# Optimization experiments

Measured on AMD Instinct MI355X. Metric: run time of the kernel, lower is better.

Reference implementation:

```python
import jax, jax.numpy as jnp
import numpy as np

B, T, C, H = 4, 2048, 768, 12
HD = C // H  # 64
EPS = 1e-5


def layer_norm(x, g, b):
    mu = jnp.mean(x, axis=-1, keepdims=True)
    var = jnp.var(x, axis=-1, keepdims=True)
    return (x - mu) * jax.lax.rsqrt(var + EPS) * g + b


def setup_inputs() -> dict:
    key = jax.random.key(0)
    ks = jax.random.split(key, 14)
    s_c = 1.0 / np.sqrt(C)
    s_4c = 1.0 / np.sqrt(4 * C)
    return {
        "x": jax.random.normal(ks[0], (B, T, C), jnp.float32),
        # per-head Q/K/V projections stacked over heads [H, C, HD]
        "wq": jax.random.uniform(ks[1], (H, C, HD), jnp.float32, -s_c, s_c),
        "bq": jnp.zeros((H, HD), jnp.float32),
        "wk": jax.random.uniform(ks[2], (H, C, HD), jnp.float32, -s_c, s_c),
        "bk": jnp.zeros((H, HD), jnp.float32),
        "wv": jax.random.uniform(ks[3], (H, C, HD), jnp.float32, -s_c, s_c),
        "bv": jnp.zeros((H, HD), jnp.float32),
        "w_proj": jax.random.uniform(ks[4], (C, C), jnp.float32, -s_c, s_c),
        "b_proj": jnp.zeros((C,), jnp.float32),
        "w1": jax.random.uniform(ks[5], (C, 4 * C), jnp.float32, -s_c, s_c),
        "b1": jnp.zeros((4 * C,), jnp.float32),
        "w2": jax.random.uniform(ks[6], (4 * C, C), jnp.float32, -s_4c, s_4c),
        "b2": jnp.zeros((C,), jnp.float32),
        "g1": jnp.ones((C,), jnp.float32),
        "beta1": jnp.zeros((C,), jnp.float32),
        "g2": jnp.ones((C,), jnp.float32),
        "beta2": jnp.zeros((C,), jnp.float32),
    }


def reference(x, wq, bq, wk, bk, wv, bv, w_proj, b_proj, w1, b1, w2, b2, g1, beta1, g2, beta2):
    # --- attention sublayer ---
    h = layer_norm(x, g1, beta1)
    q = jnp.einsum('btc,hcd->bhtd', h, wq) + bq[None, :, None, :]
    k = jnp.einsum('btc,hcd->bhtd', h, wk) + bk[None, :, None, :]
    v = jnp.einsum('btc,hcd->bhtd', h, wv) + bv[None, :, None, :]
    # NOTE: source applies NO 1/sqrt(head_size) scaling
    scores = jnp.einsum('bhtd,bhsd->bhts', q, k)  # [B,H,T,T]
    causal = jnp.tril(jnp.ones((T, T), bool))
    scores = jnp.where(causal, scores, -jnp.inf)
    wei = jax.nn.softmax(scores, axis=-1)
    attn = jnp.einsum('bhts,bhsd->bhtd', wei, v)  # [B,H,T,HD]
    attn = attn.transpose(0, 2, 1, 3).reshape(B, T, C)  # concat heads
    x = x + attn @ w_proj + b_proj
    # --- MLP sublayer ---
    h2 = layer_norm(x, g2, beta2)
    x = x + jax.nn.relu(h2 @ w1 + b1) @ w2 + b2
    return x
```

## Files before the change

### kernel.cpp

```cpp
#include <hip/hip_runtime.h>
#include <hip/hip_bf16.h>
#include <math.h>

#define BB 4
#define TT 2048
#define CC 768
#define HH 12
#define HDIM 64
#define C4 3072
#define MM (BB*TT)
#define EPSL 1e-5f

typedef __bf16 bf16x8 __attribute__((ext_vector_type(8)));
typedef float f32x4 __attribute__((ext_vector_type(4)));

__device__ __forceinline__ ushort f2bf(float f) {
    union { float f; unsigned u; } v; v.f = f;
    unsigned r = v.u + 0x7fffu + ((v.u >> 16) & 1u);
    return (ushort)(r >> 16);
}

__device__ __forceinline__ void glds16(const void* g, void* l) {
    __builtin_amdgcn_global_load_lds(
        (const __attribute__((address_space(1))) void*)g,
        (__attribute__((address_space(3))) void*)l, 16, 0, 0);
}

__global__ __launch_bounds__(256) void ln_k(const float* __restrict__ X,
                                            const float* __restrict__ G,
                                            const float* __restrict__ Be,
                                            ushort* __restrict__ O)
{
    int row = blockIdx.x;
    const float* xr = X + (size_t)row * CC;
    int t = threadIdx.x;
    float v0 = xr[t], v1 = xr[t + 256], v2 = xr[t + 512];
    float s  = v0 + v1 + v2;
    float sq = v0*v0 + v1*v1 + v2*v2;
    #pragma unroll
    for (int off = 32; off; off >>= 1) {
        s  += __shfl_xor(s,  off);
        sq += __shfl_xor(sq, off);
    }
    __shared__ float red[8];
    int wv = t >> 6, ln = t & 63;
    if (ln == 0) { red[wv] = s; red[4 + wv] = sq; }
    __syncthreads();
    s  = red[0] + red[1] + red[2] + red[3];
    sq = red[4] + red[5] + red[6] + red[7];
    float mu  = s * (1.0f / CC);
    float var = sq * (1.0f / CC) - mu * mu;
    float rs  = rsqrtf(var + EPSL);
    ushort* orow = O + (size_t)row * CC;
    orow[t]       = f2bf((v0 - mu) * rs * G[t]       + Be[t]);
    orow[t + 256] = f2bf((v1 - mu) * rs * G[t + 256] + Be[t + 256]);
    orow[t + 512] = f2bf((v2 - mu) * rs * G[t + 512] + Be[t + 512]);
}

template<int MODE>
__global__ __launch_bounds__(256) void repack_k(const float* __restrict__ W,
                                                ushort* __restrict__ WT,
                                                int K, int N, int outStride)
{
    __shared__ float tl[64][65];
    int n0 = blockIdx.x * 64, k0 = blockIdx.y * 64;
    int c = threadIdx.x & 63, rr = threadIdx.x >> 6;
    #pragma unroll
    for (int i = 0; i < 16; ++i) {
        int r = i * 4 + rr;
        float v;
        if (MODE == 0) v = W[(size_t)(k0 + r) * N + n0 + c];
        else           v = W[((size_t)(n0 >> 6) * CC + k0 + r) * 64 + c];
        tl[r][c] = v;
    }
    __syncthreads();
    #pragma unroll
    for (int i = 0; i < 16; ++i) {
        int r = i * 4 + rr;
        WT[(size_t)(n0 + r) * outStride + k0 + c] = f2bf(tl[c][r]);
    }
}

template<int EPI>
__global__ __launch_bounds__(256) void gemm_bf16(
    const ushort* __restrict__ A, const ushort* __restrict__ BT,
    int M, int N, int K,
    void* __restrict__ ov0, void* __restrict__ ov1, void* __restrict__ ov2,
    const float* __restrict__ bias0, const float* __restrict__ bias1,
    const float* __restrict__ bias2,
    const float* __restrict__ resid, ushort* __restrict__ obf)
{
    __shared__ ushort Al[128 * 32];
    __shared__ ushort Bl[128 * 32];
    int nbx = gridDim.x;
    int nwg = nbx * gridDim.y;
    int orig = blockIdx.y * nbx + blockIdx.x;
    int swz = orig;
    if ((nwg & 7) == 0) { int cpx = nwg >> 3; swz = (orig & 7) * cpx + (orig >> 3); }
    int bn = swz % nbx, bm = swz / nbx;

    int tid = threadIdx.x;
    int lane = tid & 63;
    int w = tid >> 6;
    int wr = (w >> 1) * 64, wc = (w & 1) * 64;
    int fr = lane & 15, kh = lane >> 4;

    f32x4 acc[4][4] = {};

    const size_t aRow = (size_t)bm * 128;
    const size_t bRow = (size_t)bn * 128;

    for (int k0 = 0; k0 < K; k0 += 32) {
        #pragma unroll
        for (int r = 0; r < 2; ++r) {
            int e = r * 256 + tid;
            glds16(A  + (aRow + (e >> 2)) * K + k0 + (e & 3) * 8, Al + e * 8);
            glds16(BT + (bRow + (e >> 2)) * K + k0 + (e & 3) * 8, Bl + e * 8);
        }
        __syncthreads();
        bf16x8 av[4], bv[4];
        #pragma unroll
        for (int i = 0; i < 4; ++i)
            av[i] = *(const bf16x8*)&Al[(wr + i * 16 + fr) * 32 + kh * 8];
        #pragma unroll
        for (int i = 0; i < 4; ++i)
            bv[i] = *(const bf16x8*)&Bl[(wc + i * 16 + fr) * 32 + kh * 8];
        #pragma unroll
        for (int i = 0; i < 4; ++i)
            #pragma unroll
            for (int j = 0; j < 4; ++j)
                acc[i][j] = __builtin_amdgcn_mfma_f32_16x16x32_bf16(av[i], bv[j], acc[i][j], 0, 0, 0);
        __syncthreads();
    }

    if (EPI == 1) {
        int seg = (bn * 128) / CC;
        ushort* op = (ushort*)(seg == 0 ? ov0 : (seg == 1 ? ov1 : ov2));
        const float* bsp = seg == 0 ? bias0 : (seg == 1 ? bias1 : bias2);
        int cb = bn * 128 - seg * CC + wc;
        int h = cb >> 6;
        #pragma unroll
        for (int i = 0; i < 4; ++i) {
            int row0 = bm * 128 + wr + i * 16 + kh * 4;
            int b = row0 >> 11;
            int t0 = row0 & (TT - 1);
            #pragma unroll
            for (int j = 0; j < 4; ++j) {
                int col = cb + j * 16 + fr;
                int d = col & 63;
                float bsv = bsp[col];
                #pragma unroll
                for (int r = 0; r < 4; ++r)
                    op[((size_t)(b * HH + h) * TT + t0 + r) * 64 + d] =
                        f2bf(acc[i][j][r] + bsv);
            }
        }
    } else if (EPI == 2) {
        float* o0 = (float*)ov0;
        int cb = bn * 128 + wc;
        #pragma unroll
        for (int i = 0; i < 4; ++i) {
            int row0 = bm * 128 + wr + i * 16 + kh * 4;
            #pragma unroll
            for (int j = 0; j < 4; ++j) {
                int col = cb + j * 16 + fr;
                float bsv = bias0[col];
                #pragma unroll
                for (int r = 0; r < 4; ++r) {
                    size_t idx = (size_t)(row0 + r) * N + col;
                    o0[idx] = acc[i][j][r] + bsv + resid[idx];
                }
            }
        }
    } else {
        int cb = bn * 128 + wc;
        #pragma unroll
        for (int i = 0; i < 4; ++i) {
            int row0 = bm * 128 + wr + i * 16 + kh * 4;
            #pragma unroll
            for (int j = 0; j < 4; ++j) {
                int col = cb + j * 16 + fr;
                float bsv = bias0[col];
                #pragma unroll
                for (int r = 0; r < 4; ++r) {
                    float v = fmaxf(acc[i][j][r] + bsv, 0.f);
                    obf[(size_t)(row0 + r) * N + col] = f2bf(v);
                }
            }
        }
    }
}

__global__ __launch_bounds__(256) void vtrans_k(const ushort* __restrict__ V,
                                                ushort* __restrict__ Vt)
{
    __shared__ ushort tl[64][72];
    int blk = blockIdx.x;
    int tt = blk & 31, bh = blk >> 5;
    size_t base = (size_t)bh * TT * 64;
    int t0 = tt * 64;
    int e = threadIdx.x;
    int rr = e >> 3, cc8 = (e & 7) * 8;
    #pragma unroll
    for (int p = 0; p < 2; ++p) {
        int t = p * 32 + rr;
        *(uint4*)&tl[t][cc8] = *(const uint4*)&V[base + (size_t)(t0 + t) * 64 + cc8];
    }
    __syncthreads();
    #pragma unroll
    for (int p = 0; p < 2; ++p) {
        int d = p * 32 + rr;
        ushort tmp[8];
        #pragma unroll
        for (int i = 0; i < 8; ++i) tmp[i] = tl[cc8 + i][d];
        *(uint4*)&Vt[base + (size_t)d * TT + t0 + cc8] = *(uint4*)tmp;
    }
}

__global__ __launch_bounds__(256) void attn_k(const ushort* __restrict__ Q,
                                              const ushort* __restrict__ Kb,
                                              const ushort* __restrict__ Vt,
                                              ushort* __restrict__ Ob)
{
    __shared__ ushort Kl[64][72];
    __shared__ ushort Vl[64][72];
    __shared__ ushort Pl[4][16][72];

    int orig = blockIdx.x;
    int swz = (orig & 7) * 96 + (orig >> 3);
    int pair = swz & 15;
    int bh = swz >> 4;
    int b = bh / HH, h = bh - b * HH;
    int tid = threadIdx.x, lane = tid & 63, w = tid >> 6;
    int c = lane & 15, g = lane >> 4;
    size_t base = (size_t)bh * TT * 64;
    int srow = tid >> 3, scol = (tid & 7) * 8;
    const float LOG2E = 1.44269504088896340736f;

    #pragma unroll
    for (int sel = 0; sel < 2; ++sel) {
        int qt = sel ? (31 - pair) : pair;
        int q0 = qt * 64;

        bf16x8 aq[2];
        #pragma unroll
        for (int kc = 0; kc < 2; ++kc) {
            bf16x8 raw = *(const bf16x8*)&Q[base + (size_t)(q0 + w * 16 + c) * 64 + kc * 32 + g * 8];
            #pragma unroll
            for (int e = 0; e < 8; ++e)
                raw[e] = (__bf16)((float)raw[e] * LOG2E);
            aq[kc] = raw;
        }

        f32x4 oa[4] = {};
        float mrun[4] = {-INFINITY, -INFINITY, -INFINITY, -INFINITY};
        float lrun[4] = {0.f, 0.f, 0.f, 0.f};

        for (int kv0 = 0; kv0 <= q0; kv0 += 64) {
            __syncthreads();
            #pragma unroll
            for (int p = 0; p < 2; ++p) {
                int r = p * 32 + srow;
                *(uint4*)&Kl[r][scol] = *(const uint4*)&Kb[base + (size_t)(kv0 + r) * 64 + scol];
                *(uint4*)&Vl[r][scol] = *(const uint4*)&Vt[base + (size_t)r * TT + kv0 + scol];
            }
            __syncthreads();

            f32x4 sa[4] = {};
            #pragma unroll
            for (int kc = 0; kc < 2; ++kc)
                #pragma unroll
                for (int j = 0; j < 4; ++j) {
                    bf16x8 kf = *(const bf16x8*)&Kl[j * 16 + c][kc * 32 + g * 8];
                    sa[j] = __builtin_amdgcn_mfma_f32_16x16x32_bf16(aq[kc], kf, sa[j], 0, 0, 0);
                }

            if (kv0 == q0) {
                #pragma unroll
                for (int j = 0; j < 4; ++j)
                    #pragma unroll
                    for (int r = 0; r < 4; ++r)
                        if (j * 16 + c > w * 16 + g * 4 + r) sa[j][r] = -1e30f;
            }

            float vlmax = sa[0][0];
            #pragma unroll
            for (int j = 0; j < 4; ++j)
                #pragma unroll
                for (int r = 0; r < 4; ++r) vlmax = fmaxf(vlmax, sa[j][r]);
            float mmin = fminf(fminf(mrun[0], mrun[1]), fminf(mrun[2], mrun[3]));
            if (!__all(vlmax <= mmin + 11.5f)) {
                #pragma unroll
                for (int r = 0; r < 4; ++r) {
                    float m0 = fmaxf(fmaxf(sa[0][r], sa[1][r]), fmaxf(sa[2][r], sa[3][r]));
                    #pragma unroll
                    for (int off = 8; off; off >>= 1) m0 = fmaxf(m0, __shfl_xor(m0, off));
                    float mnew = fmaxf(mrun[r], m0);
                    float sc = __builtin_amdgcn_exp2f(mrun[r] - mnew);
                    lrun[r] *= sc;
                    #pragma unroll
                    for (int j = 0; j < 4; ++j) oa[j][r] *= sc;
                    mrun[r] = mnew;
                }
            }
            #pragma unroll
            for (int r = 0; r < 4; ++r) {
                float ps = 0.f;
                #pragma unroll
                for (int j = 0; j < 4; ++j) {
                    float p = __builtin_amdgcn_exp2f(sa[j][r] - mrun[r]);
                    sa[j][r] = p;
                    ps += p;
                }
                lrun[r] += ps;
            }

            #pragma unroll
            for (int r = 0; r < 4; ++r)
                #pragma unroll
                for (int j = 0; j < 4; ++j)
                    Pl[w][g * 4 + r][j * 16 + c] = (ushort)__builtin_bit_cast(unsigned short, (__bf16)sa[j][r]);

            bf16x8 pf[2];
            #pragma unroll
            for (int kc = 0; kc < 2; ++kc)
                pf[kc] = *(const bf16x8*)&Pl[w][c][kc * 32 + g * 8];

            #pragma unroll
            for (int kc = 0; kc < 2; ++kc)
                #pragma unroll
                for (int j = 0; j < 4; ++j) {
                    bf16x8 vf = *(const bf16x8*)&Vl[j * 16 + c][kc * 32 + g * 8];
                    oa[j] = __builtin_amdgcn_mfma_f32_16x16x32_bf16(pf[kc], vf, oa[j], 0, 0, 0);
                }
        }

        float inv[4];
        #pragma unroll
        for (int r = 0; r < 4; ++r) {
            float l = lrun[r];
            #pragma unroll
            for (int off = 8; off; off >>= 1) l += __shfl_xor(l, off);
            inv[r] = 1.0f / l;
        }
        size_t orow = (size_t)b * TT + q0 + w * 16;
        #pragma unroll
        for (int j = 0; j < 4; ++j)
            #pragma unroll
            for (int r = 0; r < 4; ++r) {
                float v = oa[j][r] * inv[r];
                Ob[(orow + g * 4 + r) * CC + h * 64 + j * 16 + c] = f2bf(v);
            }
    }
}

extern "C" void kernel_launch(void* const* d_in, const int* in_sizes, int n_in,
                              void* d_out, int out_size, void* d_ws, size_t ws_size,
                              hipStream_t stream)
{
    const float* x   = (const float*)d_in[0];
    const float* wq  = (const float*)d_in[1];
    const float* bq  = (const float*)d_in[2];
    const float* wk  = (const float*)d_in[3];
    const float* bk  = (const float*)d_in[4];
    const float* wvw = (const float*)d_in[5];
    const float* bv  = (const float*)d_in[6];
    const float* wp  = (const float*)d_in[7];
    const float* bp  = (const float*)d_in[8];
    const float* w1  = (const float*)d_in[9];
    const float* b1  = (const float*)d_in[10];
    const float* w2  = (const float*)d_in[11];
    const float* b2  = (const float*)d_in[12];
    const float* g1  = (const float*)d_in[13];
    const float* be1 = (const float*)d_in[14];
    const float* g2  = (const float*)d_in[15];
    const float* be2 = (const float*)d_in[16];

    float* out = (float*)d_out;
    const size_t S = (size_t)MM * CC;

    ushort* wsu   = (ushort*)d_ws;
    ushort* WTqkv = wsu;
    ushort* WTp   = WTqkv + (size_t)2304 * 768;
    ushort* WT1   = WTp   + (size_t)768 * 768;
    ushort* WT2   = WT1   + (size_t)3072 * 768;
    ushort* hbf   = WT2   + (size_t)768 * 3072;
    ushort* attnb = hbf   + S;
    ushort* qb    = attnb + S;
    ushort* kb    = qb + S;
    ushort* vb    = kb + S;
    ushort* vtb   = vb + S;
    ushort* midb  = qb;

    dim3 rg(12, 12);
    repack_k<1><<<rg, 256, 0, stream>>>(wq,  WTqkv,                      768, 768, 768);
    repack_k<1><<<rg, 256, 0, stream>>>(wk,  WTqkv + (size_t)768*768,    768, 768, 768);
    repack_k<1><<<rg, 256, 0, stream>>>(wvw, WTqkv + (size_t)2*768*768,  768, 768, 768);
    repack_k<0><<<rg, 256, 0, stream>>>(wp,  WTp, 768, 768, 768);
    repack_k<0><<<dim3(48, 12), 256, 0, stream>>>(w1, WT1, 768, 3072, 768);
    repack_k<0><<<dim3(12, 48), 256, 0, stream>>>(w2, WT2, 3072, 768, 3072);

    ln_k<<<MM, 256, 0, stream>>>(x, g1, be1, hbf);
    gemm_bf16<1><<<dim3(18, 64), 256, 0, stream>>>(hbf, WTqkv, MM, 2304, CC,
        qb, kb, vb, bq, bk, bv, nullptr, nullptr);
    vtrans_k<<<48 * 32, 256, 0, stream>>>(vb, vtb);
    attn_k<<<48 * 16, 256, 0, stream>>>(qb, kb, vtb, attnb);
    gemm_bf16<2><<<dim3(6, 64), 256, 0, stream>>>(attnb, WTp, MM, CC, CC,
        out, nullptr, nullptr, bp, nullptr, nullptr, x, nullptr);

    ln_k<<<MM, 256, 0, stream>>>(out, g2, be2, hbf);
    gemm_bf16<3><<<dim3(24, 64), 256, 0, stream>>>(hbf, WT1, MM, C4, CC,
        nullptr, nullptr, nullptr, b1, nullptr, nullptr, nullptr, midb);
    gemm_bf16<2><<<dim3(6, 64), 256, 0, stream>>>(midb, WT2, MM, CC, C4,
        out, nullptr, nullptr, b2, nullptr, nullptr, out, nullptr);
}
```

Before: 313.6 us.

## Replace GEMM with 256x256 double-buffered 8-wave kernel using swizzled LDS

Replaces the 128x128 single-buffered bf16 GEMM with a 256x256 tile, 512-thread kernel that double-buffers K=64 slices in LDS. Each slice's global-to-LDS loads are interleaved with MFMA phases using explicit vmcnt waits and barriers. An XOR swizzle on LDS columns is meant to avoid bank conflicts. The goal is to hide global load latency behind compute and raise arithmetic intensity per tile. In exchange it uses a large LDS footprint (128KB per block), launches fewer workgroups (as few as 96 for the N=768 GEMMs, which can underfill the CUs), and relies on hand-tuned waitcnt ordering.

```diff
diff --git a/kernel.cpp b/kernel.cpp
--- a/kernel.cpp
+++ b/kernel.cpp
@@ -24,6 +24,15 @@
     __builtin_amdgcn_global_load_lds(
         (const __attribute__((address_space(1))) void*)g,
         (__attribute__((address_space(3))) void*)l, 16, 0, 0);
+}
+
+#define WVM(N) asm volatile("s_waitcnt vmcnt(" #N ")" ::: "memory")
+#define WLG0   asm volatile("s_waitcnt lgkmcnt(0)" ::: "memory")
+
+__device__ __forceinline__ void pbar() {
+    __builtin_amdgcn_sched_barrier(0);
+    __builtin_amdgcn_s_barrier();
+    __builtin_amdgcn_sched_barrier(0);
 }
 
 __global__ __launch_bounds__(256) void ln_k(const float* __restrict__ X,
@@ -82,7 +91,7 @@
 }
 
 template<int EPI>
-__global__ __launch_bounds__(256) void gemm_bf16(
+__global__ __launch_bounds__(512, 2) void gemm8p(
     const ushort* __restrict__ A, const ushort* __restrict__ BT,
     int M, int N, int K,
     void* __restrict__ ov0, void* __restrict__ ov1, void* __restrict__ ov2,
@@ -90,100 +99,152 @@
     const float* __restrict__ bias2,
     const float* __restrict__ resid, ushort* __restrict__ obf)
 {
-    __shared__ ushort Al[128 * 32];
-    __shared__ ushort Bl[128 * 32];
+    __shared__ ushort lds[2][2][256 * 64];
+
     int nbx = gridDim.x;
     int nwg = nbx * gridDim.y;
     int orig = blockIdx.y * nbx + blockIdx.x;
-    int swz = orig;
-    if ((nwg & 7) == 0) { int cpx = nwg >> 3; swz = (orig & 7) * cpx + (orig >> 3); }
+    int cpx = nwg >> 3;
+    int swz = (orig & 7) * cpx + (orig >> 3);
     int bn = swz % nbx, bm = swz / nbx;
 
     int tid = threadIdx.x;
     int lane = tid & 63;
     int w = tid >> 6;
-    int wr = (w >> 1) * 64, wc = (w & 1) * 64;
+    int wrow = (w >> 2) * 128, wcol = (w & 3) * 64;
     int fr = lane & 15, kh = lane >> 4;
-
-    f32x4 acc[4][4] = {};
-
-    const size_t aRow = (size_t)bm * 128;
-    const size_t bRow = (size_t)bn * 128;
-
-    for (int k0 = 0; k0 < K; k0 += 32) {
-        #pragma unroll
-        for (int r = 0; r < 2; ++r) {
-            int e = r * 256 + tid;
-            glds16(A  + (aRow + (e >> 2)) * K + k0 + (e & 3) * 8, Al + e * 8);
-            glds16(BT + (bRow + (e >> 2)) * K + k0 + (e & 3) * 8, Bl + e * 8);
-        }
-        __syncthreads();
-        bf16x8 av[4], bv[4];
-        #pragma unroll
-        for (int i = 0; i < 4; ++i)
-            av[i] = *(const bf16x8*)&Al[(wr + i * 16 + fr) * 32 + kh * 8];
-        #pragma unroll
-        for (int i = 0; i < 4; ++i)
-            bv[i] = *(const bf16x8*)&Bl[(wc + i * 16 + fr) * 32 + kh * 8];
-        #pragma unroll
-        for (int i = 0; i < 4; ++i)
-            #pragma unroll
-            for (int j = 0; j < 4; ++j)
-                acc[i][j] = __builtin_amdgcn_mfma_f32_16x16x32_bf16(av[i], bv[j], acc[i][j], 0, 0, 0);
-        __syncthreads();
+    int rxor = (fr & 7) * 8;
+
+    const size_t aR0 = (size_t)bm * 256;
+    const size_t bR0 = (size_t)bn * 256;
+    const int nt = K >> 6;
+
+    int srow = tid >> 3;
+    int scol = (tid & 7) * 8;
+    int gcol = scol ^ ((srow & 7) * 8);
+
+    f32x4 acc[8][4] = {};
+
+    {
+        glds16(BT + (bR0 +   0 + srow) * K + gcol, &lds[0][1][(  0 + srow) * 64 + scol]);
+        glds16(BT + (bR0 +  64 + srow) * K + gcol, &lds[0][1][( 64 + srow) * 64 + scol]);
+        glds16(BT + (bR0 + 128 + srow) * K + gcol, &lds[0][1][(128 + srow) * 64 + scol]);
+        glds16(BT + (bR0 + 192 + srow) * K + gcol, &lds[0][1][(192 + srow) * 64 + scol]);
+        glds16(A  + (aR0 +   0 + srow) * K + gcol, &lds[0][0][(  0 + srow) * 64 + scol]);
+        glds16(A  + (aR0 + 128 + srow) * K + gcol, &lds[0][0][(128 + srow) * 64 + scol]);
+        glds16(A  + (aR0 +  64 + srow) * K + gcol, &lds[0][0][( 64 + srow) * 64 + scol]);
+        glds16(A  + (aR0 + 192 + srow) * K + gcol, &lds[0][0][(192 + srow) * 64 + scol]);
+    }
+    WVM(2);
+    pbar();
+
+    for (int t = 0; t < nt; ++t) {
+        int slot = t & 1, nslot = slot ^ 1;
+        int kst = (t + 1) << 6;
+        bool st = (t + 1) < nt;
+        const ushort* Asl = &lds[slot][0][0];
+        const ushort* Bsl = &lds[slot][1][0];
+        bf16x8 aF[4][2];
+        #pragma unroll
+        for (int p = 0; p < 4; ++p) {
+            const int rh = p >> 1, ch = p & 1;
+            if (ch == 0) {
+                #pragma unroll
+                for (int i = 0; i < 4; ++i)
+                    #pragma unroll
+                    for (int k2 = 0; k2 < 2; ++k2) {
+                        int R = wrow + rh * 64 + i * 16 + fr;
+                        aF[i][k2] = *(const bf16x8*)&Asl[R * 64 + ((k2 * 32 + kh * 8) ^ rxor)];
+                    }
+            }
+            bf16x8 bF[2][2];
+            #pragma unroll
+            for (int j2 = 0; j2 < 2; ++j2)
+                #pragma unroll
+                for (int k2 = 0; k2 < 2; ++k2) {
+                    int Rb = wcol + ch * 32 + j2 * 16 + fr;
+                    bF[j2][k2] = *(const bf16x8*)&Bsl[Rb * 64 + ((k2 * 32 + kh * 8) ^ rxor)];
+                }
+            if (st) {
+                if (p == 0) {
+                    glds16(BT + (bR0 +   0 + srow) * K + kst + gcol, &lds[nslot][1][(  0 + srow) * 64 + scol]);
+                    glds16(BT + (bR0 +  64 + srow) * K + kst + gcol, &lds[nslot][1][( 64 + srow) * 64 + scol]);
+                } else if (p == 1) {
+                    glds16(BT + (bR0 + 128 + srow) * K + kst + gcol, &lds[nslot][1][(128 + srow) * 64 + scol]);
+                    glds16(BT + (bR0 + 192 + srow) * K + kst + gcol, &lds[nslot][1][(192 + srow) * 64 + scol]);
+                } else if (p == 2) {
+                    glds16(A  + (aR0 +   0 + srow) * K + kst + gcol, &lds[nslot][0][(  0 + srow) * 64 + scol]);
+                    glds16(A  + (aR0 + 128 + srow) * K + kst + gcol, &lds[nslot][0][(128 + srow) * 64 + scol]);
+                } else {
+                    glds16(A  + (aR0 +  64 + srow) * K + kst + gcol, &lds[nslot][0][( 64 + srow) * 64 + scol]);
+                    glds16(A  + (aR0 + 192 + srow) * K + kst + gcol, &lds[nslot][0][(192 + srow) * 64 + scol]);
+                }
+            }
+            __builtin_amdgcn_s_setprio(1);
+            #pragma unroll
+            for (int i = 0; i < 4; ++i)
+                #pragma unroll
+                for (int j2 = 0; j2 < 2; ++j2)
+                    #pragma unroll
+                    for (int k2 = 0; k2 < 2; ++k2)
+                        acc[rh * 4 + i][ch * 2 + j2] = __builtin_amdgcn_mfma_f32_16x16x32_bf16(
+                            aF[i][k2], bF[j2][k2], acc[rh * 4 + i][ch * 2 + j2], 0, 0, 0);
+            __builtin_amdgcn_s_setprio(0);
+            if (p == 1) { if (st) { WVM(4); } else { WVM(0); } }
+            else if (p == 3) { WVM(2); }
+            WLG0;
+            pbar();
+        }
     }
 
     if (EPI == 1) {
-        int seg = (bn * 128) / CC;
+        int seg = bn / 3;
         ushort* op = (ushort*)(seg == 0 ? ov0 : (seg == 1 ? ov1 : ov2));
         const float* bsp = seg == 0 ? bias0 : (seg == 1 ? bias1 : bias2);
-        int cb = bn * 128 - seg * CC + wc;
+        int cb = (bn - seg * 3) * 256 + wcol;
         int h = cb >> 6;
         #pragma unroll
-        for (int i = 0; i < 4; ++i) {
-            int row0 = bm * 128 + wr + i * 16 + kh * 4;
+        for (int ri = 0; ri < 8; ++ri) {
+            int row0 = bm * 256 + wrow + ri * 16 + kh * 4;
             int b = row0 >> 11;
             int t0 = row0 & (TT - 1);
             #pragma unroll
-            for (int j = 0; j < 4; ++j) {
-                int col = cb + j * 16 + fr;
-                int d = col & 63;
-                float bsv = bsp[col];
+            for (int cj = 0; cj < 4; ++cj) {
+                int d = cj * 16 + fr;
+                float bsv = bsp[h * 64 + d];
                 #pragma unroll
                 for (int r = 0; r < 4; ++r)
                     op[((size_t)(b * HH + h) * TT + t0 + r) * 64 + d] =
-                        f2bf(acc[i][j][r] + bsv);
+                        f2bf(acc[ri][cj][r] + bsv);
             }
         }
     } else if (EPI == 2) {
         float* o0 = (float*)ov0;
-        int cb = bn * 128 + wc;
-        #pragma unroll
-        for (int i = 0; i < 4; ++i) {
-            int row0 = bm * 128 + wr + i * 16 + kh * 4;
-            #pragma unroll
-            for (int j = 0; j < 4; ++j) {
-                int col = cb + j * 16 + fr;
+        #pragma unroll
+        for (int ri = 0; ri < 8; ++ri) {
+            int row0 = bm * 256 + wrow + ri * 16 + kh * 4;
+            #pragma unroll
+            for (int cj = 0; cj < 4; ++cj) {
+                int col = bn * 256 + wcol + cj * 16 + fr;
                 float bsv = bias0[col];
                 #pragma unroll
                 for (int r = 0; r < 4; ++r) {
                     size_t idx = (size_t)(row0 + r) * N + col;
-                    o0[idx] = acc[i][j][r] + bsv + resid[idx];
+                    o0[idx] = acc[ri][cj][r] + bsv + resid[idx];
                 }
             }
         }
     } else {
-        int cb = bn * 128 + wc;
-        #pragma unroll
-        for (int i = 0; i < 4; ++i) {
-            int row0 = bm * 128 + wr + i * 16 + kh * 4;
-            #pragma unroll
-            for (int j = 0; j < 4; ++j) {
-                int col = cb + j * 16 + fr;
+        #pragma unroll
+        for (int ri = 0; ri < 8; ++ri) {
+            int row0 = bm * 256 + wrow + ri * 16 + kh * 4;
+            #pragma unroll
+            for (int cj = 0; cj < 4; ++cj) {
+                int col = bn * 256 + wcol + cj * 16 + fr;
                 float bsv = bias0[col];
                 #pragma unroll
                 for (int r = 0; r < 4; ++r) {
-                    float v = fmaxf(acc[i][j][r] + bsv, 0.f);
+                    float v = fmaxf(acc[ri][cj][r] + bsv, 0.f);
                     obf[(size_t)(row0 + r) * N + col] = f2bf(v);
                 }
             }
@@ -401,16 +462,16 @@
     repack_k<0><<<dim3(12, 48), 256, 0, stream>>>(w2, WT2, 3072, 768, 3072);
 
     ln_k<<<MM, 256, 0, stream>>>(x, g1, be1, hbf);
-    gemm_bf16<1><<<dim3(18, 64), 256, 0, stream>>>(hbf, WTqkv, MM, 2304, CC,
+    gemm8p<1><<<dim3(9, 32), 512, 0, stream>>>(hbf, WTqkv, MM, 2304, CC,
         qb, kb, vb, bq, bk, bv, nullptr, nullptr);
     vtrans_k<<<48 * 32, 256, 0, stream>>>(vb, vtb);
     attn_k<<<48 * 16, 256, 0, stream>>>(qb, kb, vtb, attnb);
-    gemm_bf16<2><<<dim3(6, 64), 256, 0, stream>>>(attnb, WTp, MM, CC, CC,
+    gemm8p<2><<<dim3(3, 32), 512, 0, stream>>>(attnb, WTp, MM, CC, CC,
         out, nullptr, nullptr, bp, nullptr, nullptr, x, nullptr);
 
     ln_k<<<MM, 256, 0, stream>>>(out, g2, be2, hbf);
-    gemm_bf16<3><<<dim3(24, 64), 256, 0, stream>>>(hbf, WT1, MM, C4, CC,
+    gemm8p<3><<<dim3(12, 32), 512, 0, stream>>>(hbf, WT1, MM, C4, CC,
         nullptr, nullptr, nullptr, b1, nullptr, nullptr, nullptr, midb);
-    gemm_bf16<2><<<dim3(6, 64), 256, 0, stream>>>(midb, WT2, MM, CC, C4,
+    gemm8p<2><<<dim3(3, 32), 512, 0, stream>>>(midb, WT2, MM, CC, C4,
         out, nullptr, nullptr, b2, nullptr, nullptr, out, nullptr);
 }
```

New measurement: 316.9 us. No clear change (+1.1%).
